# Performance work log

Measured on AMD Instinct MI355X. Metric: run time of the kernel, lower is better.

Reference implementation:

```python
import jax, jax.numpy as jnp
import numpy as np

B, T, D = 32, 2048, 256
HOUT, K = 512, 8
H = HOUT // 2  # per-direction hidden


def _lstm(x, w_ih, w_hh, b_ih, b_hh):
    # x: [B,T,D]; torch gate order i,f,g,o
    b = x.shape[0]
    h0 = jnp.zeros((b, H), x.dtype)
    c0 = jnp.zeros((b, H), x.dtype)
    def step(carry, x_t):
        h, c = carry
        g = x_t @ w_ih.T + b_ih + h @ w_hh.T + b_hh
        i, f, gg, o = jnp.split(g, 4, axis=-1)
        c = jax.nn.sigmoid(f) * c + jax.nn.sigmoid(i) * jnp.tanh(gg)
        h = jax.nn.sigmoid(o) * jnp.tanh(c)
        return (h, c), h
    _, hs = jax.lax.scan(step, (h0, c0), jnp.swapaxes(x, 0, 1))
    return jnp.swapaxes(hs, 0, 1)  # [B,T,H]


def setup_inputs() -> dict:
    key = jax.random.key(0)
    ks = jax.random.split(key, 16)
    s = 0.1
    lengths = jax.random.randint(ks[1], (B,), T // 2, T + 1)
    mask = (jnp.arange(T)[None, :] < lengths[:, None])
    inp = {
        "sentences": jax.random.normal(ks[0], (B, T, D), jnp.float32),
        "tags": jax.random.randint(ks[2], (B, T), 0, K),
        "lengths": lengths,
        "mask": mask,
        # forward-direction LSTM params
        "w_ih_f": jax.random.normal(ks[3], (4 * H, D), jnp.float32) * s,
        "w_hh_f": jax.random.normal(ks[4], (4 * H, H), jnp.float32) * s,
        "b_ih_f": jax.random.normal(ks[5], (4 * H,), jnp.float32) * s,
        "b_hh_f": jax.random.normal(ks[6], (4 * H,), jnp.float32) * s,
        # backward-direction LSTM params
        "w_ih_b": jax.random.normal(ks[7], (4 * H, D), jnp.float32) * s,
        "w_hh_b": jax.random.normal(ks[8], (4 * H, H), jnp.float32) * s,
        "b_ih_b": jax.random.normal(ks[9], (4 * H,), jnp.float32) * s,
        "b_hh_b": jax.random.normal(ks[10], (4 * H,), jnp.float32) * s,
        # hidden2tag linear
        "w_tag": jax.random.normal(ks[11], (K, HOUT), jnp.float32) * s,
        "b_tag": jax.random.normal(ks[12], (K,), jnp.float32) * s,
        # CRF params
        "start_trans": jax.random.normal(ks[13], (K,), jnp.float32) * s,
        "end_trans": jax.random.normal(ks[14], (K,), jnp.float32) * s,
        "trans": jax.random.normal(ks[15], (K, K), jnp.float32) * s,
    }
    return inp


def reference(sentences, tags, lengths, mask,
              w_ih_f, w_hh_f, b_ih_f, b_hh_f,
              w_ih_b, w_hh_b, b_ih_b, b_hh_b,
              w_tag, b_tag, start_trans, end_trans, trans):
    # --- BiLSTM features (dropout is identity at eval) ---
    t_idx = jnp.arange(T)[None, :]
    L = lengths[:, None]
    rev = jnp.where(t_idx < L, L - 1 - t_idx, t_idx)  # per-sequence reversal (involution)
    x_rev = jnp.take_along_axis(sentences, rev[:, :, None], axis=1)
    h_f = _lstm(sentences, w_ih_f, w_hh_f, b_ih_f, b_hh_f)
    h_b = jnp.take_along_axis(_lstm(x_rev, w_ih_b, w_hh_b, b_ih_b, b_hh_b), rev[:, :, None], axis=1)
    feats = jnp.concatenate([h_f, h_b], axis=-1)  # [B,T,HOUT]
    emis = feats @ w_tag.T + b_tag  # [B,T,K]

    m = mask.astype(emis.dtype)
    # --- CRF numerator (gold path score) ---
    tags0 = tags[:, 0]
    num = start_trans[tags0] + jnp.take_along_axis(emis[:, 0], tags0[:, None], 1)[:, 0]
    emis_tag = jnp.take_along_axis(emis, tags[:, :, None], 2)[..., 0]  # [B,T]
    tr = trans[tags[:, :-1], tags[:, 1:]]  # [B,T-1]
    num = num + jnp.sum((tr + emis_tag[:, 1:]) * m[:, 1:], axis=1)
    last_tags = jnp.take_along_axis(tags, (lengths - 1)[:, None], 1)[:, 0]
    num = num + end_trans[last_tags]

    # --- CRF log-partition (forward algorithm, logsumexp recurrence) ---
    def step(score, inp):
        e_t, m_t = inp  # [B,K], [B]
        nxt = jax.nn.logsumexp(score[:, :, None] + trans[None] + e_t[:, None, :], axis=1)
        return jnp.where(m_t[:, None], nxt, score), None
    score0 = start_trans[None, :] + emis[:, 0]
    xs = (jnp.swapaxes(emis[:, 1:], 0, 1), jnp.swapaxes(mask[:, 1:], 0, 1))
    scoreT, _ = jax.lax.scan(step, score0, xs)
    logZ = jax.nn.logsumexp(scoreT + end_trans[None, :], axis=1)

    # reduction='mean' log-likelihood, loss = -llh
    return -jnp.mean(num - logZ)
```

## Files before the change

### kernel.cpp

```cpp
#include <hip/hip_runtime.h>


constexpr int T_ = 2048, D_ = 256, K_ = 8;

typedef __bf16 v8bf __attribute__((ext_vector_type(8)));
typedef float  v4f  __attribute__((ext_vector_type(4)));
typedef int    v8i  __attribute__((ext_vector_type(8)));
typedef unsigned int u32;
typedef unsigned long long u64;

union U64x4 { u64 q[4]; v8i v; };

__device__ __forceinline__ float sigm(float x) {
  return __builtin_amdgcn_rcpf(1.f + __expf(-x));
}
__device__ __forceinline__ float tanh_f(float x) {
  return 1.f - 2.f * __builtin_amdgcn_rcpf(__expf(2.f * x) + 1.f);
}

__device__ __forceinline__ u32 pk2bf(float a, float b) {
  union { __bf16 h[2]; u32 u; } x; x.h[0] = (__bf16)a; x.h[1] = (__bf16)b; return x.u;
}
__device__ __forceinline__ float lobf(u32 u) { union { u32 u; __bf16 h[2]; } x; x.u = u; return (float)x.h[0]; }
__device__ __forceinline__ float hibf(u32 u) { union { u32 u; __bf16 h[2]; } x; x.u = u; return (float)x.h[1]; }

__device__ __forceinline__ int gate_row(int mtg, int rr) {
  return (rr & 3) * 256 + 32 * (mtg >> 3) + 8 * (rr >> 2) + (mtg & 7);
}


__global__ __launch_bounds__(256) void prepack(
    const float* __restrict__ w_hh_f, const float* __restrict__ w_hh_b,
    const float* __restrict__ b_ih_f, const float* __restrict__ b_hh_f,
    const float* __restrict__ b_ih_b, const float* __restrict__ b_hh_b,
    const float* __restrict__ w_tag,
    u64* wh8, v8bf* wt16, float* biasp, u32* hstate_u, float* cstate)
{
  int gid = blockIdx.x * 256 + threadIdx.x;
  if (gid < 65536) {
    int lane = gid & 63, kt = (gid >> 6) & 7, mtg = (gid >> 9) & 63, d = gid >> 15;
    int rr = lane & 15, q = lane >> 4;
    const float* whh = d ? w_hh_b : w_hh_f;
    const float* src = whh + (size_t)gate_row(mtg, rr) * 256
                           + 128 * (kt >> 2) + 32 * q + 8 * (kt & 3);
    u32 lo = __builtin_amdgcn_cvt_pk_fp8_f32(src[0], src[1], 0, false);
    lo = __builtin_amdgcn_cvt_pk_fp8_f32(src[2], src[3], lo, true);
    u32 hi = __builtin_amdgcn_cvt_pk_fp8_f32(src[4], src[5], 0, false);
    hi = __builtin_amdgcn_cvt_pk_fp8_f32(src[6], src[7], hi, true);
    wh8[gid] = ((u64)hi << 32) | lo;
  } else if (gid < 66560) {
    int g = gid - 65536;
    int lane = g & 63, kt = (g >> 6) & 7, d = (g >> 9) & 1;
    int rr = lane & 15, q = lane >> 4;
    v8bf v;
    #pragma unroll
    for (int e = 0; e < 8; ++e)
      v[e] = (rr < 8) ? (__bf16)w_tag[(size_t)rr * 512 + d * 256 + 32 * kt + 8 * q + e]
                      : (__bf16)0.f;
    wt16[g] = v;
  } else if (gid < 68608) {
    int g = gid - 66560;
    int p = g & 1023, d = g >> 10;
    int gr = gate_row(p >> 4, p & 15);
    biasp[g] = (d ? b_ih_b[gr] + b_hh_b[gr] : b_ih_f[gr] + b_hh_f[gr]);
  } else if (gid < 76800) {
    hstate_u[gid - 68608] = 0u;
  } else if (gid < 93184) {
    cstate[gid - 76800] = 0.f;
  }
}

__global__ __launch_bounds__(512, 2) void fused_chunk(
    const float* __restrict__ sent, const int* __restrict__ lengths,
    const float* __restrict__ w_ih_f, const float* __restrict__ w_ih_b,
    const float* __restrict__ biasp,
    const u64* __restrict__ wh8, const v8bf* __restrict__ wt16,
    __bf16* __restrict__ hstate, float* __restrict__ cstate,
    __bf16* __restrict__ pre, __bf16* __restrict__ hbuf,
    __bf16* __restrict__ emisF, __bf16* __restrict__ emisB,
    int crec, int cpre, int cemis, int CT, int TT, int nch, int NPREB)
{
  __shared__ __align__(16) char smem[33792];

  if (blockIdx.x < 4) {
    if (crec < 0) return;
    const int s = blockIdx.x, d = s >> 1, bg = s & 1;
    const int tid = threadIdx.x, lane = tid & 63, w = tid >> 6;
    const int fm = lane & 15, q = lane >> 4;
    int Lmax = 0;
    for (int i = 0; i < 32; ++i) Lmax = max(Lmax, lengths[i]);
    const int t0 = crec * CT, t1 = t0 + CT;
    const int tend = min(t1, Lmax);

    unsigned char* h8l = (unsigned char*)smem;

    {
      int off = tid * 8, bb = off >> 8, e = off & 255;
      uint4 hv = *(const uint4*)(hstate + (size_t)s * 4096 + off);
      float f0 = lobf(hv.x), f1 = hibf(hv.x), f2 = lobf(hv.y), f3 = hibf(hv.y);
      float f4 = lobf(hv.z), f5 = hibf(hv.z), f6 = lobf(hv.w), f7 = hibf(hv.w);
      u32 lo = __builtin_amdgcn_cvt_pk_fp8_f32(f0, f1, 0, false);
      lo = __builtin_amdgcn_cvt_pk_fp8_f32(f2, f3, lo, true);
      u32 hi = __builtin_amdgcn_cvt_pk_fp8_f32(f4, f5, 0, false);
      hi = __builtin_amdgcn_cvt_pk_fp8_f32(f6, f7, hi, true);
      *(u64*)&h8l[4352 + bb * 272 + e] = ((u64)hi << 32) | lo;
    }

    v8i afr0[8], afr1[8];
    #pragma unroll
    for (int mt = 0; mt < 8; ++mt) {
      int mtg = 8 * w + mt;
      U64x4 lo, hi;
      #pragma unroll
      for (int jj = 0; jj < 4; ++jj) {
        lo.q[jj] = wh8[((size_t)(d * 64 + mtg) * 8 + jj) * 64 + lane];
        hi.q[jj] = wh8[((size_t)(d * 64 + mtg) * 8 + 4 + jj) * 64 + lane];
      }
      afr0[mt] = lo.v; afr1[mt] = hi.v;
    }
    float c8[8];
    #pragma unroll
    for (int mt = 0; mt < 8; ++mt) c8[mt] = cstate[((size_t)s * 512 + tid) * 8 + mt];

    const char* preBase = (const char*)pre + (size_t)(crec & 1) * CT * 131072;
    __bf16* hslot = hbuf + ((size_t)(crec & 1) * 2 + d) * CT * 8192;

    uint2 pA[8];
    {
      const char* pb = preBase + (((size_t)d * CT * 32 + (bg * 16 + fm)) * 1024) * 2;
      #pragma unroll
      for (int mt = 0; mt < 8; ++mt)
        pA[mt] = *(const uint2*)(pb + (16 * (8 * w + mt) + 4 * q) * 2);
    }

    uint4 hv4;
    hv4.x = 0u; hv4.y = 0u; hv4.z = 0u; hv4.w = 0u;

    for (int t = t0; t < tend; ++t) {
      asm volatile("s_waitcnt lgkmcnt(0)" ::: "memory");
      __builtin_amdgcn_s_barrier();

      v4f acc[8];
      #pragma unroll
      for (int mt = 0; mt < 8; ++mt)
        acc[mt] = v4f{lobf(pA[mt].x), hibf(pA[mt].x), lobf(pA[mt].y), hibf(pA[mt].y)};
      v4f accb[8];
      #pragma unroll
      for (int mt = 0; mt < 8; ++mt) accb[mt] = v4f{0.f, 0.f, 0.f, 0.f};

      uint2 pN[8];
      {
        int tn = min(t + 1, tend - 1);
        const char* pb = preBase +
            ((((size_t)d * CT + (tn - t0)) * 32 + (bg * 16 + fm)) * 1024) * 2;
        #pragma unroll
        for (int mt = 0; mt < 8; ++mt)
          pN[mt] = *(const uint2*)(pb + (16 * (8 * w + mt) + 4 * q) * 2);
      }

      const int pp = (t + 1) & 1;
      v8i b0 = *(const v8i*)&h8l[pp * 4352 + fm * 272 + 32 * q];
      v8i b1 = *(const v8i*)&h8l[pp * 4352 + fm * 272 + 128 + 32 * q];

      #pragma unroll
      for (int mt = 0; mt < 8; ++mt)
        acc[mt] = __builtin_amdgcn_mfma_scale_f32_16x16x128_f8f6f4(
            afr0[mt], b0, acc[mt], 0, 0, 0, 0x7f7f7f7f, 0, 0x7f7f7f7f);
      #pragma unroll
      for (int mt = 0; mt < 8; ++mt)
        accb[mt] = __builtin_amdgcn_mfma_scale_f32_16x16x128_f8f6f4(
            afr1[mt], b1, accb[mt], 0, 0, 0, 0x7f7f7f7f, 0, 0x7f7f7f7f);

      float hh[8];
      #pragma unroll
      for (int mt = 0; mt < 8; ++mt) {
        float gi = acc[mt][0] + accb[mt][0];
        float gf = acc[mt][1] + accb[mt][1];
        float gg = acc[mt][2] + accb[mt][2];
        float go = acc[mt][3] + accb[mt][3];
        float c = sigm(gf) * c8[mt] + sigm(gi) * tanh_f(gg);
        c8[mt] = c;
        hh[mt] = sigm(go) * tanh_f(c);
      }

      {
        u32 lo = __builtin_amdgcn_cvt_pk_fp8_f32(hh[0], hh[1], 0, false);
        lo = __builtin_amdgcn_cvt_pk_fp8_f32(hh[2], hh[3], lo, true);
        u32 hi = __builtin_amdgcn_cvt_pk_fp8_f32(hh[4], hh[5], 0, false);
        hi = __builtin_amdgcn_cvt_pk_fp8_f32(hh[6], hh[7], hi, true);
        *(u64*)&h8l[(t & 1) * 4352 + fm * 272 + 32 * w + 8 * q] = ((u64)hi << 32) | lo;
      }
      hv4.x = pk2bf(hh[0], hh[1]); hv4.y = pk2bf(hh[2], hh[3]);
      hv4.z = pk2bf(hh[4], hh[5]); hv4.w = pk2bf(hh[6], hh[7]);
      *(uint4*)(hslot + ((size_t)(t - t0) * 32 + bg * 16 + fm) * 256 + 32 * w + 8 * q) = hv4;

      #pragma unroll
      for (int mt = 0; mt < 8; ++mt) pA[mt] = pN[mt];
    }

    if (tend > t0) {
      #pragma unroll
      for (int mt = 0; mt < 8; ++mt) cstate[((size_t)s * 512 + tid) * 8 + mt] = c8[mt];
      *(uint4*)(hstate + (size_t)s * 4096 + fm * 256 + 32 * w + 8 * q) = hv4;
    }
    return;
  }

  if ((int)blockIdx.x < 4 + NPREB) {
    if (cpre >= nch) return;
    const int u = (blockIdx.x - 4) * 2 + (threadIdx.x >> 8);
    const int b = u & 31, d = (u >> 5) & 1, zz = u >> 6;
    const int tg = zz >> 2, rg = zz & 3;
    const int tid = threadIdx.x & 255, lane = tid & 63, w = tid >> 6;
    const int fm = lane & 15, q = lane >> 4;
    const int NT = TT >> 4;
    const int t0 = cpre * CT;
    const int Lb = lengths[b];
    const float* wih = d ? w_ih_b : w_ih_f;
    __bf16* xl = (__bf16*)(smem + (threadIdx.x >> 8) * 16896);
    __bf16* preS = pre + (size_t)(cpre & 1) * CT * 65536;

    for (int rep = 0; rep < NT; ++rep) {
      int tl = (tid >> 4) + 16 * rep, c16 = (tid & 15) * 16;
      int tglob = t0 + TT * tg + tl;
      int pos = d ? ((tglob < Lb) ? (Lb - 1 - tglob) : tglob) : tglob;
      const float4* xp = (const float4*)(sent + ((size_t)b * T_ + pos) * D_ + c16);
      float4 a0 = xp[0], a1 = xp[1], a2 = xp[2], a3 = xp[3];
      v8bf v0, v1;
      v0[0]=(__bf16)a0.x; v0[1]=(__bf16)a0.y; v0[2]=(__bf16)a0.z; v0[3]=(__bf16)a0.w;
      v0[4]=(__bf16)a1.x; v0[5]=(__bf16)a1.y; v0[6]=(__bf16)a1.z; v0[7]=(__bf16)a1.w;
      v1[0]=(__bf16)a2.x; v1[1]=(__bf16)a2.y; v1[2]=(__bf16)a2.z; v1[3]=(__bf16)a2.w;
      v1[4]=(__bf16)a3.x; v1[5]=(__bf16)a3.y; v1[6]=(__bf16)a3.z; v1[7]=(__bf16)a3.w;
      *(v8bf*)&xl[tl * 264 + c16]     = v0;
      *(v8bf*)&xl[tl * 264 + c16 + 8] = v1;
    }

    v8bf af[4][8];
    v4f acc[4][2];
    #pragma unroll
    for (int mt = 0; mt < 4; ++mt) {
      int mtg = 16 * rg + 4 * w + mt;
      const float* src = wih + (size_t)gate_row(mtg, fm) * 256 + 8 * q;
      #pragma unroll
      for (int kt = 0; kt < 8; ++kt) {
        float4 a = *(const float4*)(src + 32 * kt);
        float4 b2 = *(const float4*)(src + 32 * kt + 4);
        v8bf v;
        v[0]=(__bf16)a.x;  v[1]=(__bf16)a.y;  v[2]=(__bf16)a.z;  v[3]=(__bf16)a.w;
        v[4]=(__bf16)b2.x; v[5]=(__bf16)b2.y; v[6]=(__bf16)b2.z; v[7]=(__bf16)b2.w;
        af[mt][kt] = v;
      }
      float4 bs = *(const float4*)(biasp + d * 1024 + 16 * mtg + 4 * q);
      for (int nt = 0; nt < 2; ++nt) acc[mt][nt] = v4f{bs.x, bs.y, bs.z, bs.w};
    }
    __syncthreads();

    for (int kt = 0; kt < 8; ++kt) {
      for (int nt = 0; nt < NT; ++nt) {
        v8bf bfr = *(const v8bf*)&xl[(nt * 16 + fm) * 264 + 32 * kt + 8 * q];
        #pragma unroll
        for (int mt = 0; mt < 4; ++mt)
          acc[mt][nt] = __builtin_amdgcn_mfma_f32_16x16x32_bf16(af[mt][kt], bfr, acc[mt][nt], 0, 0, 0);
      }
    }

    #pragma unroll
    for (int mt = 0; mt < 4; ++mt) {
      int mtg = 16 * rg + 4 * w + mt;
      for (int nt = 0; nt < NT; ++nt) {
        int tl = TT * tg + nt * 16 + fm;
        uint2 pk;
        pk.x = pk2bf(acc[mt][nt][0], acc[mt][nt][1]);
        pk.y = pk2bf(acc[mt][nt][2], acc[mt][nt][3]);
        size_t off = (((size_t)d * CT + tl) * 32 + b) * 1024 + 16 * mtg + 4 * q;
        *(uint2*)((char*)preS + off * 2) = pk;
      }
    }
    return;
  }

  if (cemis < 0) return;
  {
    const int eb = blockIdx.x - 4 - NPREB;
    const int u = eb * 8 + (threadIdx.x >> 6);
    const int b = u & 31, d2 = (u >> 5) & 1, tg2 = u >> 6;
    if (tg2 >= CT / 16) return;
    const int lane = threadIdx.x & 63, fm = lane & 15, q = lane >> 4;
    const int Ln = lengths[b];
    const int tl = tg2 * 16 + fm;
    const __bf16* hrow = hbuf + ((((size_t)(cemis & 1) * 2 + d2) * CT + tl) * 32 + b) * 256;
    v4f ea = {0.f, 0.f, 0.f, 0.f};
    #pragma unroll
    for (int kt = 0; kt < 8; ++kt) {
      v8bf wa = wt16[((size_t)d2 * 8 + kt) * 64 + lane];
      v8bf hb = *(const v8bf*)(hrow + 32 * kt + 8 * q);
      ea = __builtin_amdgcn_mfma_f32_16x16x32_bf16(wa, hb, ea, 0, 0, 0);
    }
    int se = cemis * CT + tl;
    if (q < 2 && se < Ln) {
      int pos = d2 ? (Ln - 1 - se) : se;
      __bf16* emis = d2 ? emisB : emisF;
      uint2 pk; pk.x = pk2bf(ea[0], ea[1]); pk.y = pk2bf(ea[2], ea[3]);
      *(uint2*)((char*)emis + (((size_t)b * T_ + pos) * K_ + 4 * q) * 2) = pk;
    }
  }
}

__global__ __launch_bounds__(64) void crf_pass(
    const int* __restrict__ lengths, const int* __restrict__ tags,
    const float* __restrict__ b_tag, const float* __restrict__ start_trans,
    const float* __restrict__ end_trans, const float* __restrict__ trans,
    const __bf16* __restrict__ emisF, const __bf16* __restrict__ emisB, float* out)
{
  int b = blockIdx.x;
  int l = threadIdx.x;
  int L = lengths[b];
  int j = l >> 3, k = l & 7;
  float trl = trans[j * 8 + k];
  float btk = b_tag[k];
  const __bf16* eF = emisF + (size_t)b * T_ * K_;
  const __bf16* eB = emisB + (size_t)b * T_ * K_;
  const uint4* pF = (const uint4*)eF;
  const uint4* pB = (const uint4*)eB;

  __shared__ float buf[2][64][16];
  {
    uint4 uF = pF[l], uB = pB[l];
    float* r = &buf[0][l][0];
    r[0]=lobf(uF.x); r[1]=hibf(uF.x); r[2]=lobf(uF.y); r[3]=hibf(uF.y);
    r[4]=lobf(uF.z); r[5]=hibf(uF.z); r[6]=lobf(uF.w); r[7]=hibf(uF.w);
    r[8]=lobf(uB.x); r[9]=hibf(uB.x); r[10]=lobf(uB.y); r[11]=hibf(uB.y);
    r[12]=lobf(uB.z); r[13]=hibf(uB.z); r[14]=lobf(uB.w); r[15]=hibf(uB.w);
  }
  __syncthreads();

  float score = start_trans[j] + buf[0][0][j] + buf[0][0][8 + j] + b_tag[j];
  int nch = (L + 63) >> 6;
  for (int c = 0; c < nch; ++c) {
    uint4 preF, preB;
    bool more = (c + 1 < nch);
    if (more) { preF = pF[64 * (c + 1) + l]; preB = pB[64 * (c + 1) + l]; }
    int cur = c & 1;
    int tendc = min(64, L - 64 * c);
    for (int tt = (c == 0 ? 1 : 0); tt < tendc; ++tt) {
      float e = buf[cur][tt][k] + buf[cur][tt][8 + k] + btk;
      float m = __shfl(score, 0);
      float p = __expf(score + trl - m);
      p += __shfl_xor(p, 8); p += __shfl_xor(p, 16); p += __shfl_xor(p, 32);
      score = __shfl(m + __logf(p) + e, j);
    }
    if (more) {
      __syncthreads();
      float* r = &buf[cur ^ 1][l][0];
      r[0]=lobf(preF.x); r[1]=hibf(preF.x); r[2]=lobf(preF.y); r[3]=hibf(preF.y);
      r[4]=lobf(preF.z); r[5]=hibf(preF.z); r[6]=lobf(preF.w); r[7]=hibf(preF.w);
      r[8]=lobf(preB.x); r[9]=hibf(preB.x); r[10]=lobf(preB.y); r[11]=hibf(preB.y);
      r[12]=lobf(preB.z); r[13]=hibf(preB.z); r[14]=lobf(preB.w); r[15]=hibf(preB.w);
      __syncthreads();
    }
  }

  float v = score + end_trans[j];
  float m = fmaxf(v, __shfl_xor(v, 8)); m = fmaxf(m, __shfl_xor(m, 16)); m = fmaxf(m, __shfl_xor(m, 32));
  float p = __expf(v - m);
  p += __shfl_xor(p, 8); p += __shfl_xor(p, 16); p += __shfl_xor(p, 32);
  float logZ = m + __logf(p);

  const int* tg = tags + (size_t)b * T_;
  float nsum = 0.f;
  for (int t = l; t < L; t += 64) {
    int tt = tg[t];
    float e = (float)eF[t * 8 + tt] + (float)eB[t * 8 + tt] + b_tag[tt];
    float tr = (t > 0) ? trans[tg[t - 1] * 8 + tt] : 0.f;
    nsum += e + tr;
  }
  nsum += __shfl_xor(nsum, 1);  nsum += __shfl_xor(nsum, 2);  nsum += __shfl_xor(nsum, 4);
  nsum += __shfl_xor(nsum, 8);  nsum += __shfl_xor(nsum, 16); nsum += __shfl_xor(nsum, 32);
  if (l == 0) {
    float num = nsum + start_trans[tg[0]] + end_trans[tg[L - 1]];
    atomicAdd(out, (logZ - num) * (1.f / 32.f));
  }
}

extern "C" void kernel_launch(void* const* d_in, const int* in_sizes, int n_in,
                              void* d_out, int out_size, void* d_ws, size_t ws_size,
                              hipStream_t stream) {
  (void)in_sizes; (void)n_in; (void)out_size;
  const float* sent        = (const float*)d_in[0];
  const int*   tags        = (const int*)d_in[1];
  const int*   lengths     = (const int*)d_in[2];
  const float* w_ih_f      = (const float*)d_in[4];
  const float* w_hh_f      = (const float*)d_in[5];
  const float* b_ih_f      = (const float*)d_in[6];
  const float* b_hh_f      = (const float*)d_in[7];
  const float* w_ih_b      = (const float*)d_in[8];
  const float* w_hh_b      = (const float*)d_in[9];
  const float* b_ih_b      = (const float*)d_in[10];
  const float* b_hh_b      = (const float*)d_in[11];
  const float* w_tag       = (const float*)d_in[12];
  const float* b_tag       = (const float*)d_in[13];
  const float* start_trans = (const float*)d_in[14];
  const float* end_trans   = (const float*)d_in[15];
  const float* trans       = (const float*)d_in[16];

  char* ws = (char*)d_ws;
  u64*    wh8    = (u64*)(ws + 0x000000);
  v8bf*   wt16   = (v8bf*)(ws + 0x080000);
  float*  biasp  = (float*)(ws + 0x084000);
  __bf16* hstate = (__bf16*)(ws + 0x086000);
  float*  cstate = (float*)(ws + 0x08E000);
  __bf16* emisF  = (__bf16*)(ws + 0x100000);
  __bf16* emisB  = (__bf16*)(ws + 0x200000);
  __bf16* pre    = (__bf16*)(ws + 0x300000);

  int CT = 64;
  for (int cand : {256, 128}) {
    if ((size_t)0x300000 + (size_t)cand * (2 * 131072 + 2 * 32768) <= ws_size) { CT = cand; break; }
  }
  __bf16* hbuf = (__bf16*)(ws + 0x300000 + 2ull * (size_t)CT * 131072ull);
  const int TT = 32;
  const int nch = T_ / CT;
  const int NPREB = 128 * (CT / TT);
  const int NEMIS = CT / 2;
  dim3 grid(4 + NPREB + NEMIS, 1, 1);

  hipMemsetAsync(d_out, 0, sizeof(float), stream);
  prepack<<<364, 256, 0, stream>>>(w_hh_f, w_hh_b, b_ih_f, b_hh_f, b_ih_b, b_hh_b,
                                   w_tag, wh8, wt16, biasp, (u32*)hstate, cstate);
  fused_chunk<<<grid, 512, 0, stream>>>(sent, lengths, w_ih_f, w_ih_b, biasp, wh8, wt16,
                                        hstate, cstate, pre, hbuf, emisF, emisB,
                                        -1, 0, -1, CT, TT, nch, NPREB);
  for (int c = 0; c < nch; ++c)
    fused_chunk<<<grid, 512, 0, stream>>>(sent, lengths, w_ih_f, w_ih_b, biasp, wh8, wt16,
                                          hstate, cstate, pre, hbuf, emisF, emisB,
                                          c, c + 1, c - 1, CT, TT, nch, NPREB);
  fused_chunk<<<grid, 512, 0, stream>>>(sent, lengths, w_ih_f, w_ih_b, biasp, wh8, wt16,
                                        hstate, cstate, pre, hbuf, emisF, emisB,
                                        -1, nch, nch - 1, CT, TT, nch, NPREB);
  crf_pass<<<32, 64, 0, stream>>>(lengths, tags, b_tag, start_trans, end_trans, trans,
                                  emisF, emisB, (float*)d_out);
}
```

Baseline: 4.350 ms.

## Double recurrent block to 1024 threads, halving per-thread LSTM gate tiles

Launches the fused chunk kernel with 1024 threads so each recurrent wave owns 4 gate tiles instead of 8, shortening the serial per-timestep MFMA and activation chain on the latency-bound LSTM recurrence. The projection blocks idle their upper half and stream W_ih per k-slice instead of holding it all in registers, and emission blocks process 16 waves each. This trades heavier barrier cost across 16 waves per step and wasted lanes in the projection blocks for less work per thread on the critical path.

```diff
diff --git a/kernel.cpp b/kernel.cpp
--- a/kernel.cpp
+++ b/kernel.cpp
@@ -70,7 +70,7 @@
   }
 }
 
-__global__ __launch_bounds__(512, 2) void fused_chunk(
+__global__ __launch_bounds__(1024) void fused_chunk(
     const float* __restrict__ sent, const int* __restrict__ lengths,
     const float* __restrict__ w_ih_f, const float* __restrict__ w_ih_b,
     const float* __restrict__ biasp,
@@ -87,6 +87,7 @@
     const int s = blockIdx.x, d = s >> 1, bg = s & 1;
     const int tid = threadIdx.x, lane = tid & 63, w = tid >> 6;
     const int fm = lane & 15, q = lane >> 4;
+    const int e4 = 32 * (w >> 1) + 8 * q + 4 * (w & 1);
     int Lmax = 0;
     for (int i = 0; i < 32; ++i) Lmax = max(Lmax, lengths[i]);
     const int t0 = crec * CT, t1 = t0 + CT;
@@ -95,21 +96,16 @@
     unsigned char* h8l = (unsigned char*)smem;
 
     {
-      int off = tid * 8, bb = off >> 8, e = off & 255;
-      uint4 hv = *(const uint4*)(hstate + (size_t)s * 4096 + off);
-      float f0 = lobf(hv.x), f1 = hibf(hv.x), f2 = lobf(hv.y), f3 = hibf(hv.y);
-      float f4 = lobf(hv.z), f5 = hibf(hv.z), f6 = lobf(hv.w), f7 = hibf(hv.w);
-      u32 lo = __builtin_amdgcn_cvt_pk_fp8_f32(f0, f1, 0, false);
-      lo = __builtin_amdgcn_cvt_pk_fp8_f32(f2, f3, lo, true);
-      u32 hi = __builtin_amdgcn_cvt_pk_fp8_f32(f4, f5, 0, false);
-      hi = __builtin_amdgcn_cvt_pk_fp8_f32(f6, f7, hi, true);
-      *(u64*)&h8l[4352 + bb * 272 + e] = ((u64)hi << 32) | lo;
-    }
-
-    v8i afr0[8], afr1[8];
-    #pragma unroll
-    for (int mt = 0; mt < 8; ++mt) {
-      int mtg = 8 * w + mt;
+      uint2 hv = *(const uint2*)(hstate + (size_t)s * 4096 + fm * 256 + e4);
+      u32 pk8 = __builtin_amdgcn_cvt_pk_fp8_f32(lobf(hv.x), hibf(hv.x), 0, false);
+      pk8 = __builtin_amdgcn_cvt_pk_fp8_f32(lobf(hv.y), hibf(hv.y), pk8, true);
+      *(u32*)&h8l[4352 + fm * 272 + e4] = pk8;
+    }
+
+    v8i afr0[4], afr1[4];
+    #pragma unroll
+    for (int mt = 0; mt < 4; ++mt) {
+      int mtg = 4 * w + mt;
       U64x4 lo, hi;
       #pragma unroll
       for (int jj = 0; jj < 4; ++jj) {
@@ -118,62 +114,55 @@
       }
       afr0[mt] = lo.v; afr1[mt] = hi.v;
     }
-    float c8[8];
-    #pragma unroll
-    for (int mt = 0; mt < 8; ++mt) c8[mt] = cstate[((size_t)s * 512 + tid) * 8 + mt];
+    float c8[4];
+    #pragma unroll
+    for (int mt = 0; mt < 4; ++mt) c8[mt] = cstate[((size_t)s * 1024 + tid) * 4 + mt];
 
     const char* preBase = (const char*)pre + (size_t)(crec & 1) * CT * 131072;
     __bf16* hslot = hbuf + ((size_t)(crec & 1) * 2 + d) * CT * 8192;
-
-    uint2 pA[8];
-    {
-      const char* pb = preBase + (((size_t)d * CT * 32 + (bg * 16 + fm)) * 1024) * 2;
-      #pragma unroll
-      for (int mt = 0; mt < 8; ++mt)
-        pA[mt] = *(const uint2*)(pb + (16 * (8 * w + mt) + 4 * q) * 2);
-    }
-
-    uint4 hv4;
-    hv4.x = 0u; hv4.y = 0u; hv4.z = 0u; hv4.w = 0u;
+    const char* pb0 = preBase + (((size_t)d * CT * 32 + (bg * 16 + fm)) * 1024
+                                 + 16 * (4 * w) + 4 * q) * 2;
+
+    uint2 pA[4];
+    #pragma unroll
+    for (int mt = 0; mt < 4; ++mt)
+      pA[mt] = *(const uint2*)(pb0 + 32 * mt);
 
     for (int t = t0; t < tend; ++t) {
       asm volatile("s_waitcnt lgkmcnt(0)" ::: "memory");
       __builtin_amdgcn_s_barrier();
 
-      v4f acc[8];
-      #pragma unroll
-      for (int mt = 0; mt < 8; ++mt)
-        acc[mt] = v4f{lobf(pA[mt].x), hibf(pA[mt].x), lobf(pA[mt].y), hibf(pA[mt].y)};
-      v4f accb[8];
-      #pragma unroll
-      for (int mt = 0; mt < 8; ++mt) accb[mt] = v4f{0.f, 0.f, 0.f, 0.f};
-
-      uint2 pN[8];
-      {
-        int tn = min(t + 1, tend - 1);
-        const char* pb = preBase +
-            ((((size_t)d * CT + (tn - t0)) * 32 + (bg * 16 + fm)) * 1024) * 2;
-        #pragma unroll
-        for (int mt = 0; mt < 8; ++mt)
-          pN[mt] = *(const uint2*)(pb + (16 * (8 * w + mt) + 4 * q) * 2);
-      }
-
       const int pp = (t + 1) & 1;
       v8i b0 = *(const v8i*)&h8l[pp * 4352 + fm * 272 + 32 * q];
       v8i b1 = *(const v8i*)&h8l[pp * 4352 + fm * 272 + 128 + 32 * q];
 
-      #pragma unroll
-      for (int mt = 0; mt < 8; ++mt)
+      v4f acc[4], accb[4];
+      #pragma unroll
+      for (int mt = 0; mt < 4; ++mt) {
+        acc[mt] = v4f{lobf(pA[mt].x), hibf(pA[mt].x), lobf(pA[mt].y), hibf(pA[mt].y)};
+        accb[mt] = v4f{0.f, 0.f, 0.f, 0.f};
+      }
+
+      {
+        int tn = min(t + 1, tend - 1);
+        const char* pb = pb0 + (size_t)(tn - t0) * 65536;
+        #pragma unroll
+        for (int mt = 0; mt < 4; ++mt)
+          pA[mt] = *(const uint2*)(pb + 32 * mt);
+      }
+
+      #pragma unroll
+      for (int mt = 0; mt < 4; ++mt)
         acc[mt] = __builtin_amdgcn_mfma_scale_f32_16x16x128_f8f6f4(
             afr0[mt], b0, acc[mt], 0, 0, 0, 0x7f7f7f7f, 0, 0x7f7f7f7f);
       #pragma unroll
-      for (int mt = 0; mt < 8; ++mt)
+      for (int mt = 0; mt < 4; ++mt)
         accb[mt] = __builtin_amdgcn_mfma_scale_f32_16x16x128_f8f6f4(
             afr1[mt], b1, accb[mt], 0, 0, 0, 0x7f7f7f7f, 0, 0x7f7f7f7f);
 
-      float hh[8];
-      #pragma unroll
-      for (int mt = 0; mt < 8; ++mt) {
+      float hh[4];
+      #pragma unroll
+      for (int mt = 0; mt < 4; ++mt) {
         float gi = acc[mt][0] + accb[mt][0];
         float gf = acc[mt][1] + accb[mt][1];
         float gg = acc[mt][2] + accb[mt][2];
@@ -184,30 +173,29 @@
       }
 
       {
-        u32 lo = __builtin_amdgcn_cvt_pk_fp8_f32(hh[0], hh[1], 0, false);
-        lo = __builtin_amdgcn_cvt_pk_fp8_f32(hh[2], hh[3], lo, true);
-        u32 hi = __builtin_amdgcn_cvt_pk_fp8_f32(hh[4], hh[5], 0, false);
-        hi = __builtin_amdgcn_cvt_pk_fp8_f32(hh[6], hh[7], hi, true);
-        *(u64*)&h8l[(t & 1) * 4352 + fm * 272 + 32 * w + 8 * q] = ((u64)hi << 32) | lo;
-      }
-      hv4.x = pk2bf(hh[0], hh[1]); hv4.y = pk2bf(hh[2], hh[3]);
-      hv4.z = pk2bf(hh[4], hh[5]); hv4.w = pk2bf(hh[6], hh[7]);
-      *(uint4*)(hslot + ((size_t)(t - t0) * 32 + bg * 16 + fm) * 256 + 32 * w + 8 * q) = hv4;
-
-      #pragma unroll
-      for (int mt = 0; mt < 8; ++mt) pA[mt] = pN[mt];
+        u32 pk8 = __builtin_amdgcn_cvt_pk_fp8_f32(hh[0], hh[1], 0, false);
+        pk8 = __builtin_amdgcn_cvt_pk_fp8_f32(hh[2], hh[3], pk8, true);
+        *(u32*)&h8l[(t & 1) * 4352 + fm * 272 + e4] = pk8;
+      }
+      {
+        uint2 hv;
+        hv.x = pk2bf(hh[0], hh[1]); hv.y = pk2bf(hh[2], hh[3]);
+        *(uint2*)(hslot + ((size_t)(t - t0) * 32 + bg * 16 + fm) * 256 + e4) = hv;
+        if (t == tend - 1)
+          *(uint2*)(hstate + (size_t)s * 4096 + fm * 256 + e4) = hv;
+      }
     }
 
     if (tend > t0) {
       #pragma unroll
-      for (int mt = 0; mt < 8; ++mt) cstate[((size_t)s * 512 + tid) * 8 + mt] = c8[mt];
-      *(uint4*)(hstate + (size_t)s * 4096 + fm * 256 + 32 * w + 8 * q) = hv4;
+      for (int mt = 0; mt < 4; ++mt) cstate[((size_t)s * 1024 + tid) * 4 + mt] = c8[mt];
     }
     return;
   }
 
   if ((int)blockIdx.x < 4 + NPREB) {
     if (cpre >= nch) return;
+    const bool act = threadIdx.x < 512;
     const int u = (blockIdx.x - 4) * 2 + (threadIdx.x >> 8);
     const int b = u & 31, d = (u >> 5) & 1, zz = u >> 6;
     const int tg = zz >> 2, rg = zz & 3;
@@ -215,52 +203,54 @@
     const int fm = lane & 15, q = lane >> 4;
     const int NT = TT >> 4;
     const int t0 = cpre * CT;
-    const int Lb = lengths[b];
     const float* wih = d ? w_ih_b : w_ih_f;
     __bf16* xl = (__bf16*)(smem + (threadIdx.x >> 8) * 16896);
     __bf16* preS = pre + (size_t)(cpre & 1) * CT * 65536;
 
-    for (int rep = 0; rep < NT; ++rep) {
-      int tl = (tid >> 4) + 16 * rep, c16 = (tid & 15) * 16;
-      int tglob = t0 + TT * tg + tl;
-      int pos = d ? ((tglob < Lb) ? (Lb - 1 - tglob) : tglob) : tglob;
-      const float4* xp = (const float4*)(sent + ((size_t)b * T_ + pos) * D_ + c16);
-      float4 a0 = xp[0], a1 = xp[1], a2 = xp[2], a3 = xp[3];
-      v8bf v0, v1;
-      v0[0]=(__bf16)a0.x; v0[1]=(__bf16)a0.y; v0[2]=(__bf16)a0.z; v0[3]=(__bf16)a0.w;
-      v0[4]=(__bf16)a1.x; v0[5]=(__bf16)a1.y; v0[6]=(__bf16)a1.z; v0[7]=(__bf16)a1.w;
-      v1[0]=(__bf16)a2.x; v1[1]=(__bf16)a2.y; v1[2]=(__bf16)a2.z; v1[3]=(__bf16)a2.w;
-      v1[4]=(__bf16)a3.x; v1[5]=(__bf16)a3.y; v1[6]=(__bf16)a3.z; v1[7]=(__bf16)a3.w;
-      *(v8bf*)&xl[tl * 264 + c16]     = v0;
-      *(v8bf*)&xl[tl * 264 + c16 + 8] = v1;
-    }
-
-    v8bf af[4][8];
+    if (act) {
+      const int Lb = lengths[b];
+      for (int rep = 0; rep < NT; ++rep) {
+        int tl = (tid >> 4) + 16 * rep, c16 = (tid & 15) * 16;
+        int tglob = t0 + TT * tg + tl;
+        int pos = d ? ((tglob < Lb) ? (Lb - 1 - tglob) : tglob) : tglob;
+        const float4* xp = (const float4*)(sent + ((size_t)b * T_ + pos) * D_ + c16);
+        float4 a0 = xp[0], a1 = xp[1], a2 = xp[2], a3 = xp[3];
+        v8bf v0, v1;
+        v0[0]=(__bf16)a0.x; v0[1]=(__bf16)a0.y; v0[2]=(__bf16)a0.z; v0[3]=(__bf16)a0.w;
+        v0[4]=(__bf16)a1.x; v0[5]=(__bf16)a1.y; v0[6]=(__bf16)a1.z; v0[7]=(__bf16)a1.w;
+        v1[0]=(__bf16)a2.x; v1[1]=(__bf16)a2.y; v1[2]=(__bf16)a2.z; v1[3]=(__bf16)a2.w;
+        v1[4]=(__bf16)a3.x; v1[5]=(__bf16)a3.y; v1[6]=(__bf16)a3.z; v1[7]=(__bf16)a3.w;
+        *(v8bf*)&xl[tl * 264 + c16]     = v0;
+        *(v8bf*)&xl[tl * 264 + c16 + 8] = v1;
+      }
+    }
+    __syncthreads();
+    if (!act) return;
+
     v4f acc[4][2];
     #pragma unroll
     for (int mt = 0; mt < 4; ++mt) {
-      int mtg = 16 * rg + 4 * w + mt;
-      const float* src = wih + (size_t)gate_row(mtg, fm) * 256 + 8 * q;
-      #pragma unroll
-      for (int kt = 0; kt < 8; ++kt) {
-        float4 a = *(const float4*)(src + 32 * kt);
-        float4 b2 = *(const float4*)(src + 32 * kt + 4);
+      float4 bs = *(const float4*)(biasp + d * 1024 + 16 * (16 * rg + 4 * w + mt) + 4 * q);
+      for (int nt = 0; nt < 2; ++nt) acc[mt][nt] = v4f{bs.x, bs.y, bs.z, bs.w};
+    }
+
+    for (int kt = 0; kt < 8; ++kt) {
+      v8bf af[4];
+      #pragma unroll
+      for (int mt = 0; mt < 4; ++mt) {
+        const float* src = wih + (size_t)gate_row(16 * rg + 4 * w + mt, fm) * 256 + 8 * q + 32 * kt;
+        float4 a = *(const float4*)(src);
+        float4 b2 = *(const float4*)(src + 4);
         v8bf v;
         v[0]=(__bf16)a.x;  v[1]=(__bf16)a.y;  v[2]=(__bf16)a.z;  v[3]=(__bf16)a.w;
         v[4]=(__bf16)b2.x; v[5]=(__bf16)b2.y; v[6]=(__bf16)b2.z; v[7]=(__bf16)b2.w;
-        af[mt][kt] = v;
-      }
-      float4 bs = *(const float4*)(biasp + d * 1024 + 16 * mtg + 4 * q);
-      for (int nt = 0; nt < 2; ++nt) acc[mt][nt] = v4f{bs.x, bs.y, bs.z, bs.w};
-    }
-    __syncthreads();
-
-    for (int kt = 0; kt < 8; ++kt) {
+        af[mt] = v;
+      }
       for (int nt = 0; nt < NT; ++nt) {
         v8bf bfr = *(const v8bf*)&xl[(nt * 16 + fm) * 264 + 32 * kt + 8 * q];
         #pragma unroll
         for (int mt = 0; mt < 4; ++mt)
-          acc[mt][nt] = __builtin_amdgcn_mfma_f32_16x16x32_bf16(af[mt][kt], bfr, acc[mt][nt], 0, 0, 0);
+          acc[mt][nt] = __builtin_amdgcn_mfma_f32_16x16x32_bf16(af[mt], bfr, acc[mt][nt], 0, 0, 0);
       }
     }
 
@@ -282,7 +272,7 @@
   if (cemis < 0) return;
   {
     const int eb = blockIdx.x - 4 - NPREB;
-    const int u = eb * 8 + (threadIdx.x >> 6);
+    const int u = eb * 16 + (threadIdx.x >> 6);
     const int b = u & 31, d2 = (u >> 5) & 1, tg2 = u >> 6;
     if (tg2 >= CT / 16) return;
     const int lane = threadIdx.x & 63, fm = lane & 15, q = lane >> 4;
@@ -421,22 +411,22 @@
   const int TT = 32;
   const int nch = T_ / CT;
   const int NPREB = 128 * (CT / TT);
-  const int NEMIS = CT / 2;
+  const int NEMIS = CT / 4;
   dim3 grid(4 + NPREB + NEMIS, 1, 1);
 
   hipMemsetAsync(d_out, 0, sizeof(float), stream);
   prepack<<<364, 256, 0, stream>>>(w_hh_f, w_hh_b, b_ih_f, b_hh_f, b_ih_b, b_hh_b,
                                    w_tag, wh8, wt16, biasp, (u32*)hstate, cstate);
-  fused_chunk<<<grid, 512, 0, stream>>>(sent, lengths, w_ih_f, w_ih_b, biasp, wh8, wt16,
-                                        hstate, cstate, pre, hbuf, emisF, emisB,
-                                        -1, 0, -1, CT, TT, nch, NPREB);
+  fused_chunk<<<grid, 1024, 0, stream>>>(sent, lengths, w_ih_f, w_ih_b, biasp, wh8, wt16,
+                                         hstate, cstate, pre, hbuf, emisF, emisB,
+                                         -1, 0, -1, CT, TT, nch, NPREB);
   for (int c = 0; c < nch; ++c)
-    fused_chunk<<<grid, 512, 0, stream>>>(sent, lengths, w_ih_f, w_ih_b, biasp, wh8, wt16,
-                                          hstate, cstate, pre, hbuf, emisF, emisB,
-                                          c, c + 1, c - 1, CT, TT, nch, NPREB);
-  fused_chunk<<<grid, 512, 0, stream>>>(sent, lengths, w_ih_f, w_ih_b, biasp, wh8, wt16,
-                                        hstate, cstate, pre, hbuf, emisF, emisB,
-                                        -1, nch, nch - 1, CT, TT, nch, NPREB);
+    fused_chunk<<<grid, 1024, 0, stream>>>(sent, lengths, w_ih_f, w_ih_b, biasp, wh8, wt16,
+                                           hstate, cstate, pre, hbuf, emisF, emisB,
+                                           c, c + 1, c - 1, CT, TT, nch, NPREB);
+  fused_chunk<<<grid, 1024, 0, stream>>>(sent, lengths, w_ih_f, w_ih_b, biasp, wh8, wt16,
+                                         hstate, cstate, pre, hbuf, emisF, emisB,
+                                         -1, nch, nch - 1, CT, TT, nch, NPREB);
   crf_pass<<<32, 64, 0, stream>>>(lengths, tags, b_tag, start_trans, end_trans, trans,
                                   emisF, emisB, (float*)d_out);
 }
```

Measured after the change: 4.440 ms. 2.1% more time.
